# Performance work log

Hardware: AMD Instinct MI355X
Metric: run time of the kernel (lower is better)

The kernel has to match this reference:

```python
import jax, jax.numpy as jnp
import numpy as np

N_NODES = 100000
N_EDGES = 3200000
D_FEAT = 64


def setup_inputs() -> dict:
    key = jax.random.key(0)
    k1, k2, k3 = jax.random.split(key, 3)
    x = jax.random.normal(k1, (N_NODES, D_FEAT), dtype=jnp.float32)
    up_index = jax.random.randint(k2, (2, N_EDGES), 0, N_NODES, dtype=jnp.int64)
    down_index = jax.random.randint(k3, (2, N_EDGES), 0, N_NODES, dtype=jnp.int64)
    return {"x": x, "up_index": up_index, "down_index": down_index}


def _propagate(x, edge_index, num_nodes):
    # flow = 'source_to_target': (i, j) = (1, 0)
    # __lift__: gather x along node_dim=-2 at source indices (row j=0)
    msg = x[edge_index[0]]                      # [E, D]  message_up(x_j) = x_j
    # aggregate 'add': scatter-add messages to target indices (row i=1)
    return jax.ops.segment_sum(msg, edge_index[1], num_segments=num_nodes)  # [N, D]


def reference(x, up_index, down_index):
    up_out = _propagate(x, up_index, x.shape[0])
    down_out = _propagate(x, down_index, x.shape[0])
    # update: combine up and down aggregations (identity update -> sum)
    return up_out + down_out
```

## Files before the change

### kernel.cpp

```cpp
#include <hip/hip_runtime.h>


static constexpr int D = 64;
static constexpr int Q = 16;
static constexpr int NPB = 64;
static constexpr int NPB_SHIFT = 6;
static constexpr int CHUNK = 16384;
static constexpr int CH = 4096;

__global__ void detect_idx_dtype(const int* __restrict__ w, int* __restrict__ flag) {
    int tid = threadIdx.x;
    int v = w[2 * tid + 1];
    unsigned long long m = __ballot(v != 0);
    if (tid == 0) *flag = (m == 0ULL) ? 1 : 0;
}

__device__ __forceinline__ int load_idx(const void* idx, long long i, int is64) {
    return is64 ? (int)((const long long*)idx)[i] : ((const int*)idx)[i];
}

__global__ __launch_bounds__(256) void bucket_hist_kernel(
        const void* __restrict__ up, const void* __restrict__ down,
        int* __restrict__ bcounts, const int* __restrict__ flag, int E, int NB) {
    extern __shared__ int lcnt[];
    const int is64 = *flag;
    for (int i = threadIdx.x; i < NB; i += blockDim.x) lcnt[i] = 0;
    __syncthreads();
    const long long total = 2LL * E;
    const long long stride = (long long)gridDim.x * blockDim.x;
    for (long long e = (long long)blockIdx.x * blockDim.x + threadIdx.x;
         e < total; e += stride) {
        const void* idx = up; long long ee = e;
        if (ee >= E) { idx = down; ee -= E; }
        int dst = load_idx(idx, E + ee, is64);
        atomicAdd(&lcnt[dst >> NPB_SHIFT], 1);
    }
    __syncthreads();
    for (int i = threadIdx.x; i < NB; i += blockDim.x)
        if (lcnt[i]) atomicAdd(&bcounts[i], lcnt[i]);
}

__global__ __launch_bounds__(1024) void scan_kernel(
        const int* __restrict__ counts, int* __restrict__ offsets,
        int* __restrict__ cursors, int NB) {
    __shared__ int sums[1024];
    const int tid = threadIdx.x;
    const int chunk = (NB + 1023) / 1024;
    const int start = tid * chunk;
    const int end = min(start + chunk, NB);
    int s = 0;
    for (int i = start; i < end; i++) s += counts[i];
    sums[tid] = s;
    __syncthreads();
    for (int off = 1; off < 1024; off <<= 1) {
        int t = (tid >= off) ? sums[tid - off] : 0;
        __syncthreads();
        sums[tid] += t;
        __syncthreads();
    }
    int run = (tid == 0) ? 0 : sums[tid - 1];
    for (int i = start; i < end; i++) {
        offsets[i] = run;
        cursors[i] = run;
        run += counts[i];
    }
    if (tid == 1023) offsets[NB] = run;
}

__global__ __launch_bounds__(256) void bucket_scatter_kernel(
        const void* __restrict__ up, const void* __restrict__ down,
        int* __restrict__ gcursor, unsigned* __restrict__ packed,
        const int* __restrict__ flag, int E, int NB) {
    extern __shared__ int lds[];
    int* cnt = lds;
    int* base = lds + NB;
    const int is64 = *flag;
    const long long total = 2LL * E;
    const long long cs = (long long)blockIdx.x * CHUNK;
    if (cs >= total) return;
    const long long ce = min(total, cs + (long long)CHUNK);

    for (int i = threadIdx.x; i < NB; i += blockDim.x) cnt[i] = 0;
    __syncthreads();
    for (long long e = cs + threadIdx.x; e < ce; e += blockDim.x) {
        const void* idx = up; long long ee = e;
        if (ee >= E) { idx = down; ee -= E; }
        int dst = load_idx(idx, E + ee, is64);
        atomicAdd(&cnt[dst >> NPB_SHIFT], 1);
    }
    __syncthreads();
    for (int i = threadIdx.x; i < NB; i += blockDim.x) {
        int c = cnt[i];
        base[i] = c ? atomicAdd(&gcursor[i], c) : 0;
        cnt[i] = 0;
    }
    __syncthreads();
    for (long long e = cs + threadIdx.x; e < ce; e += blockDim.x) {
        const void* idx = up; long long ee = e;
        if (ee >= E) { idx = down; ee -= E; }
        int src = load_idx(idx, ee, is64);
        int dst = load_idx(idx, E + ee, is64);
        int b = dst >> NPB_SHIFT;
        int pos = base[b] + atomicAdd(&cnt[b], 1);
        packed[pos] = ((unsigned)src << NPB_SHIFT) | (unsigned)(dst & (NPB - 1));
    }
}

__global__ __launch_bounds__(256) void bucket_gather_kernel(
        const float* __restrict__ x, const int* __restrict__ offsets,
        const unsigned* __restrict__ packed, float* __restrict__ out, int N) {
    __shared__ unsigned sorted[CH];
    __shared__ int cnt[NPB];
    __shared__ int binoff[NPB + 1];
    __shared__ int cursor[NPB];

    const int b = blockIdx.x;
    const int tid = threadIdx.x;
    const int g = tid >> 4;
    const int q = tid & 15;
    const int beg = offsets[b], end = offsets[b + 1];

    float4 acc[4];
    acc[0] = acc[1] = acc[2] = acc[3] = make_float4(0.f, 0.f, 0.f, 0.f);

    for (int cs = beg; cs < end; cs += CH) {
        const int m = min(CH, end - cs);
        for (int i = tid; i < NPB; i += 256) cnt[i] = 0;
        __syncthreads();
        for (int i = tid; i < m; i += 256)
            atomicAdd(&cnt[packed[cs + i] & (NPB - 1)], 1);
        __syncthreads();
        if (tid < NPB) {
            int v = cnt[tid];
            int inc = v;
            #pragma unroll
            for (int off = 1; off < 64; off <<= 1) {
                int t = __shfl_up(inc, off, 64);
                if (tid >= off) inc += t;
            }
            binoff[tid + 1] = inc;
            cursor[tid] = inc - v;
            if (tid == 0) binoff[0] = 0;
        }
        __syncthreads();
        for (int i = tid; i < m; i += 256) {
            unsigned p = packed[cs + i];
            int pos = atomicAdd(&cursor[p & (NPB - 1)], 1);
            sorted[pos] = p;
        }
        __syncthreads();
        #pragma unroll
        for (int j = 0; j < 4; j++) {
            const int dl = 4 * g + j;
            const int rb = binoff[dl], re = binoff[dl + 1];
            int e = rb;
            for (; e + 3 < re; e += 4) {
                unsigned p0 = sorted[e], p1 = sorted[e + 1];
                unsigned p2 = sorted[e + 2], p3 = sorted[e + 3];
                const float4 v0 = *(const float4*)(x + ((long long)(p0 >> NPB_SHIFT)) * D + q * 4);
                const float4 v1 = *(const float4*)(x + ((long long)(p1 >> NPB_SHIFT)) * D + q * 4);
                const float4 v2 = *(const float4*)(x + ((long long)(p2 >> NPB_SHIFT)) * D + q * 4);
                const float4 v3 = *(const float4*)(x + ((long long)(p3 >> NPB_SHIFT)) * D + q * 4);
                acc[j].x += (v0.x + v1.x) + (v2.x + v3.x);
                acc[j].y += (v0.y + v1.y) + (v2.y + v3.y);
                acc[j].z += (v0.z + v1.z) + (v2.z + v3.z);
                acc[j].w += (v0.w + v1.w) + (v2.w + v3.w);
            }
            for (; e < re; e++) {
                unsigned p = sorted[e];
                const float4 v = *(const float4*)(x + ((long long)(p >> NPB_SHIFT)) * D + q * 4);
                acc[j].x += v.x; acc[j].y += v.y; acc[j].z += v.z; acc[j].w += v.w;
            }
        }
        __syncthreads();
    }

    const int node0 = b * NPB;
    #pragma unroll
    for (int j = 0; j < 4; j++) {
        const int node = node0 + 4 * g + j;
        if (node < N)
            *(float4*)(out + (long long)node * D + q * 4) = acc[j];
    }
}

__global__ __launch_bounds__(256) void scatter_add_kernel(
        const float* __restrict__ x, const void* __restrict__ up_idx,
        const void* __restrict__ down_idx, float* __restrict__ out,
        const int* __restrict__ dtype_flag, int num_edges) {
    const int is64 = *dtype_flag;
    const long long total = 2LL * num_edges * Q;
    const long long stride = (long long)gridDim.x * blockDim.x;
    for (long long t = (long long)blockIdx.x * blockDim.x + threadIdx.x;
         t < total; t += stride) {
        const int quad = (int)(t & (Q - 1));
        long long eg = t >> 4;
        const void* idx = up_idx;
        if (eg >= num_edges) { idx = down_idx; eg -= num_edges; }
        int src = load_idx(idx, eg, is64);
        int dst = load_idx(idx, num_edges + eg, is64);
        const float4 v = *(const float4*)(x + (long long)src * D + quad * 4);
        float* o = out + (long long)dst * D + quad * 4;
        unsafeAtomicAdd(o + 0, v.x);
        unsafeAtomicAdd(o + 1, v.y);
        unsafeAtomicAdd(o + 2, v.z);
        unsafeAtomicAdd(o + 3, v.w);
    }
}

extern "C" void kernel_launch(void* const* d_in, const int* in_sizes, int n_in,
                              void* d_out, int out_size, void* d_ws, size_t ws_size,
                              hipStream_t stream) {
    const float* x = (const float*)d_in[0];
    const void* up_idx = d_in[1];
    const void* down_idx = d_in[2];
    float* out = (float*)d_out;

    const int E = in_sizes[1] / 2;
    const int N = out_size / D;
    const int NB = (N + NPB - 1) / NPB;
    const long long Etot = 2LL * E;

    int* ws_i = (int*)d_ws;
    int* flag = ws_i;
    int* counts = ws_i + 64;
    int* offsets = counts + NB;
    int* cursors = offsets + NB + 15;
    unsigned* packed = (unsigned*)(cursors + NB);
    const size_t ws_need = (size_t)(64 + 3LL * NB + 16 + Etot) * 4 + 64;

    detect_idx_dtype<<<1, 64, 0, stream>>>((const int*)up_idx, flag);

    if (ws_size >= ws_need && N <= (1 << 25) && Etot < (1LL << 31)) {
        hipMemsetAsync(counts, 0, (size_t)NB * sizeof(int), stream);
        bucket_hist_kernel<<<512, 256, NB * sizeof(int), stream>>>(
            up_idx, down_idx, counts, flag, E, NB);
        scan_kernel<<<1, 1024, 0, stream>>>(counts, offsets, cursors, NB);
        const int sblocks = (int)((Etot + CHUNK - 1) / CHUNK);
        bucket_scatter_kernel<<<sblocks, 256, 2 * NB * sizeof(int), stream>>>(
            up_idx, down_idx, cursors, packed, flag, E, NB);
        bucket_gather_kernel<<<NB, 256, 0, stream>>>(x, offsets, packed, out, N);
    } else {
        hipMemsetAsync(d_out, 0, (size_t)out_size * sizeof(float), stream);
        scatter_add_kernel<<<8192, 256, 0, stream>>>(x, up_idx, down_idx, out, flag, E);
    }
}
```

Baseline: 496.5 us.

## Replace bucketed two-level sort with full per-node CSR counting sort

Replaces the 64-node bucket sort and in-block LDS re-sort with a full per-destination counting sort. It histograms with global atomics per node, runs a two-pass multi-block scan, and scatters source indices into CSR order. The gather kernel then reads each node's contiguous source list directly, unrolled by 8, with nontemporal index loads and no shared memory or barriers. This removes the LDS sorting stage and the serial single-block scan, at the cost of heavy contention on global atomics in the hist and scatter passes and a fully random scatter write pattern.

```diff
diff --git a/kernel.cpp b/kernel.cpp
--- a/kernel.cpp
+++ b/kernel.cpp
@@ -3,10 +3,8 @@
 
 static constexpr int D = 64;
 static constexpr int Q = 16;
-static constexpr int NPB = 64;
-static constexpr int NPB_SHIFT = 6;
-static constexpr int CHUNK = 16384;
-static constexpr int CH = 4096;
+static constexpr int NPB = 32;
+static constexpr int SB = 256;
 
 __global__ void detect_idx_dtype(const int* __restrict__ w, int* __restrict__ flag) {
     int tid = threadIdx.x;
@@ -19,13 +17,10 @@
     return is64 ? (int)((const long long*)idx)[i] : ((const int*)idx)[i];
 }
 
-__global__ __launch_bounds__(256) void bucket_hist_kernel(
+__global__ __launch_bounds__(256) void hist_kernel(
         const void* __restrict__ up, const void* __restrict__ down,
-        int* __restrict__ bcounts, const int* __restrict__ flag, int E, int NB) {
-    extern __shared__ int lcnt[];
+        int* __restrict__ counts, const int* __restrict__ flag, int E) {
     const int is64 = *flag;
-    for (int i = threadIdx.x; i < NB; i += blockDim.x) lcnt[i] = 0;
-    __syncthreads();
     const long long total = 2LL * E;
     const long long stride = (long long)gridDim.x * blockDim.x;
     for (long long e = (long long)blockIdx.x * blockDim.x + threadIdx.x;
@@ -33,154 +28,134 @@
         const void* idx = up; long long ee = e;
         if (ee >= E) { idx = down; ee -= E; }
         int dst = load_idx(idx, E + ee, is64);
-        atomicAdd(&lcnt[dst >> NPB_SHIFT], 1);
-    }
-    __syncthreads();
-    for (int i = threadIdx.x; i < NB; i += blockDim.x)
-        if (lcnt[i]) atomicAdd(&bcounts[i], lcnt[i]);
-}
-
-__global__ __launch_bounds__(1024) void scan_kernel(
-        const int* __restrict__ counts, int* __restrict__ offsets,
-        int* __restrict__ cursors, int NB) {
-    __shared__ int sums[1024];
-    const int tid = threadIdx.x;
-    const int chunk = (NB + 1023) / 1024;
-    const int start = tid * chunk;
-    const int end = min(start + chunk, NB);
+        atomicAdd(&counts[dst], 1);
+    }
+}
+
+__global__ __launch_bounds__(256) void scan_partials_kernel(
+        const int* __restrict__ counts, int* __restrict__ partials,
+        int N, int cpt) {
+    __shared__ int red[256];
+    const int blk = blockIdx.x, tid = threadIdx.x;
+    const long long base = (long long)(blk * 256 + tid) * cpt;
     int s = 0;
-    for (int i = start; i < end; i++) s += counts[i];
-    sums[tid] = s;
-    __syncthreads();
-    for (int off = 1; off < 1024; off <<= 1) {
-        int t = (tid >= off) ? sums[tid - off] : 0;
-        __syncthreads();
-        sums[tid] += t;
-        __syncthreads();
-    }
-    int run = (tid == 0) ? 0 : sums[tid - 1];
-    for (int i = start; i < end; i++) {
-        offsets[i] = run;
-        cursors[i] = run;
-        run += counts[i];
-    }
-    if (tid == 1023) offsets[NB] = run;
-}
-
-__global__ __launch_bounds__(256) void bucket_scatter_kernel(
+    for (int k = 0; k < cpt; k++) {
+        long long i = base + k;
+        if (i < N) s += counts[i];
+    }
+    red[tid] = s;
+    __syncthreads();
+    for (int off = 128; off > 0; off >>= 1) {
+        if (tid < off) red[tid] += red[tid + off];
+        __syncthreads();
+    }
+    if (tid == 0) partials[blk] = red[0];
+}
+
+__global__ __launch_bounds__(256) void scan_apply_kernel(
+        const int* __restrict__ counts, const int* __restrict__ partials,
+        int* __restrict__ offsets, int* __restrict__ cursors,
+        int N, int cpt, int total) {
+    __shared__ int sh[256];
+    const int blk = blockIdx.x, tid = threadIdx.x;
+    sh[tid] = (tid < blk) ? partials[tid] : 0;
+    __syncthreads();
+    for (int off = 128; off > 0; off >>= 1) {
+        if (tid < off) sh[tid] += sh[tid + off];
+        __syncthreads();
+    }
+    const int bbase = sh[0];
+    __syncthreads();
+    const long long base = (long long)(blk * 256 + tid) * cpt;
+    int s = 0;
+    for (int k = 0; k < cpt; k++) {
+        long long i = base + k;
+        if (i < N) s += counts[i];
+    }
+    sh[tid] = s;
+    __syncthreads();
+    for (int off = 1; off < 256; off <<= 1) {
+        int t = (tid >= off) ? sh[tid - off] : 0;
+        __syncthreads();
+        sh[tid] += t;
+        __syncthreads();
+    }
+    int run = bbase + ((tid == 0) ? 0 : sh[tid - 1]);
+    for (int k = 0; k < cpt; k++) {
+        long long i = base + k;
+        if (i < N) {
+            int c = counts[i];
+            offsets[i] = run;
+            cursors[i] = run;
+            run += c;
+        }
+    }
+    if (blk == 0 && tid == 0) offsets[N] = total;
+}
+
+__global__ __launch_bounds__(256) void scatter_kernel(
         const void* __restrict__ up, const void* __restrict__ down,
-        int* __restrict__ gcursor, unsigned* __restrict__ packed,
-        const int* __restrict__ flag, int E, int NB) {
-    extern __shared__ int lds[];
-    int* cnt = lds;
-    int* base = lds + NB;
+        int* __restrict__ cursors, int* __restrict__ srcbuf,
+        const int* __restrict__ flag, int E) {
     const int is64 = *flag;
     const long long total = 2LL * E;
-    const long long cs = (long long)blockIdx.x * CHUNK;
-    if (cs >= total) return;
-    const long long ce = min(total, cs + (long long)CHUNK);
-
-    for (int i = threadIdx.x; i < NB; i += blockDim.x) cnt[i] = 0;
-    __syncthreads();
-    for (long long e = cs + threadIdx.x; e < ce; e += blockDim.x) {
-        const void* idx = up; long long ee = e;
-        if (ee >= E) { idx = down; ee -= E; }
-        int dst = load_idx(idx, E + ee, is64);
-        atomicAdd(&cnt[dst >> NPB_SHIFT], 1);
-    }
-    __syncthreads();
-    for (int i = threadIdx.x; i < NB; i += blockDim.x) {
-        int c = cnt[i];
-        base[i] = c ? atomicAdd(&gcursor[i], c) : 0;
-        cnt[i] = 0;
-    }
-    __syncthreads();
-    for (long long e = cs + threadIdx.x; e < ce; e += blockDim.x) {
+    const long long stride = (long long)gridDim.x * blockDim.x;
+    for (long long e = (long long)blockIdx.x * blockDim.x + threadIdx.x;
+         e < total; e += stride) {
         const void* idx = up; long long ee = e;
         if (ee >= E) { idx = down; ee -= E; }
         int src = load_idx(idx, ee, is64);
         int dst = load_idx(idx, E + ee, is64);
-        int b = dst >> NPB_SHIFT;
-        int pos = base[b] + atomicAdd(&cnt[b], 1);
-        packed[pos] = ((unsigned)src << NPB_SHIFT) | (unsigned)(dst & (NPB - 1));
-    }
-}
-
-__global__ __launch_bounds__(256) void bucket_gather_kernel(
+        int pos = atomicAdd(&cursors[dst], 1);
+        __builtin_nontemporal_store(src, &srcbuf[pos]);
+    }
+}
+
+__global__ __launch_bounds__(256, 6) void gather_kernel(
         const float* __restrict__ x, const int* __restrict__ offsets,
-        const unsigned* __restrict__ packed, float* __restrict__ out, int N) {
-    __shared__ unsigned sorted[CH];
-    __shared__ int cnt[NPB];
-    __shared__ int binoff[NPB + 1];
-    __shared__ int cursor[NPB];
-
-    const int b = blockIdx.x;
+        const int* __restrict__ srcs, float* __restrict__ out, int N) {
     const int tid = threadIdx.x;
     const int g = tid >> 4;
     const int q = tid & 15;
-    const int beg = offsets[b], end = offsets[b + 1];
-
-    float4 acc[4];
-    acc[0] = acc[1] = acc[2] = acc[3] = make_float4(0.f, 0.f, 0.f, 0.f);
-
-    for (int cs = beg; cs < end; cs += CH) {
-        const int m = min(CH, end - cs);
-        for (int i = tid; i < NPB; i += 256) cnt[i] = 0;
-        __syncthreads();
-        for (int i = tid; i < m; i += 256)
-            atomicAdd(&cnt[packed[cs + i] & (NPB - 1)], 1);
-        __syncthreads();
-        if (tid < NPB) {
-            int v = cnt[tid];
-            int inc = v;
-            #pragma unroll
-            for (int off = 1; off < 64; off <<= 1) {
-                int t = __shfl_up(inc, off, 64);
-                if (tid >= off) inc += t;
-            }
-            binoff[tid + 1] = inc;
-            cursor[tid] = inc - v;
-            if (tid == 0) binoff[0] = 0;
-        }
-        __syncthreads();
-        for (int i = tid; i < m; i += 256) {
-            unsigned p = packed[cs + i];
-            int pos = atomicAdd(&cursor[p & (NPB - 1)], 1);
-            sorted[pos] = p;
-        }
-        __syncthreads();
-        #pragma unroll
-        for (int j = 0; j < 4; j++) {
-            const int dl = 4 * g + j;
-            const int rb = binoff[dl], re = binoff[dl + 1];
+    const float* xq = x + q * 4;
+
+    #pragma unroll
+    for (int j = 0; j < 2; j++) {
+        const int node = blockIdx.x * NPB + 2 * g + j;
+        if (node < N) {
+            const int rb = offsets[node];
+            const int re = offsets[node + 1];
+            float4 acc = make_float4(0.f, 0.f, 0.f, 0.f);
             int e = rb;
-            for (; e + 3 < re; e += 4) {
-                unsigned p0 = sorted[e], p1 = sorted[e + 1];
-                unsigned p2 = sorted[e + 2], p3 = sorted[e + 3];
-                const float4 v0 = *(const float4*)(x + ((long long)(p0 >> NPB_SHIFT)) * D + q * 4);
-                const float4 v1 = *(const float4*)(x + ((long long)(p1 >> NPB_SHIFT)) * D + q * 4);
-                const float4 v2 = *(const float4*)(x + ((long long)(p2 >> NPB_SHIFT)) * D + q * 4);
-                const float4 v3 = *(const float4*)(x + ((long long)(p3 >> NPB_SHIFT)) * D + q * 4);
-                acc[j].x += (v0.x + v1.x) + (v2.x + v3.x);
-                acc[j].y += (v0.y + v1.y) + (v2.y + v3.y);
-                acc[j].z += (v0.z + v1.z) + (v2.z + v3.z);
-                acc[j].w += (v0.w + v1.w) + (v2.w + v3.w);
+            for (; e + 8 <= re; e += 8) {
+                const int s0 = __builtin_nontemporal_load(srcs + e + 0);
+                const int s1 = __builtin_nontemporal_load(srcs + e + 1);
+                const int s2 = __builtin_nontemporal_load(srcs + e + 2);
+                const int s3 = __builtin_nontemporal_load(srcs + e + 3);
+                const int s4 = __builtin_nontemporal_load(srcs + e + 4);
+                const int s5 = __builtin_nontemporal_load(srcs + e + 5);
+                const int s6 = __builtin_nontemporal_load(srcs + e + 6);
+                const int s7 = __builtin_nontemporal_load(srcs + e + 7);
+                const float4 v0 = *(const float4*)(xq + (long long)s0 * D);
+                const float4 v1 = *(const float4*)(xq + (long long)s1 * D);
+                const float4 v2 = *(const float4*)(xq + (long long)s2 * D);
+                const float4 v3 = *(const float4*)(xq + (long long)s3 * D);
+                const float4 v4 = *(const float4*)(xq + (long long)s4 * D);
+                const float4 v5 = *(const float4*)(xq + (long long)s5 * D);
+                const float4 v6 = *(const float4*)(xq + (long long)s6 * D);
+                const float4 v7 = *(const float4*)(xq + (long long)s7 * D);
+                acc.x += ((v0.x + v1.x) + (v2.x + v3.x)) + ((v4.x + v5.x) + (v6.x + v7.x));
+                acc.y += ((v0.y + v1.y) + (v2.y + v3.y)) + ((v4.y + v5.y) + (v6.y + v7.y));
+                acc.z += ((v0.z + v1.z) + (v2.z + v3.z)) + ((v4.z + v5.z) + (v6.z + v7.z));
+                acc.w += ((v0.w + v1.w) + (v2.w + v3.w)) + ((v4.w + v5.w) + (v6.w + v7.w));
             }
             for (; e < re; e++) {
-                unsigned p = sorted[e];
-                const float4 v = *(const float4*)(x + ((long long)(p >> NPB_SHIFT)) * D + q * 4);
-                acc[j].x += v.x; acc[j].y += v.y; acc[j].z += v.z; acc[j].w += v.w;
+                const int s = __builtin_nontemporal_load(srcs + e);
+                const float4 v = *(const float4*)(xq + (long long)s * D);
+                acc.x += v.x; acc.y += v.y; acc.z += v.z; acc.w += v.w;
             }
+            *(float4*)(out + (long long)node * D + q * 4) = acc;
         }
-        __syncthreads();
-    }
-
-    const int node0 = b * NPB;
-    #pragma unroll
-    for (int j = 0; j < 4; j++) {
-        const int node = node0 + 4 * g + j;
-        if (node < N)
-            *(float4*)(out + (long long)node * D + q * 4) = acc[j];
     }
 }
 
@@ -218,28 +193,29 @@
 
     const int E = in_sizes[1] / 2;
     const int N = out_size / D;
-    const int NB = (N + NPB - 1) / NPB;
     const long long Etot = 2LL * E;
 
     int* ws_i = (int*)d_ws;
     int* flag = ws_i;
     int* counts = ws_i + 64;
-    int* offsets = counts + NB;
-    int* cursors = offsets + NB + 15;
-    unsigned* packed = (unsigned*)(cursors + NB);
-    const size_t ws_need = (size_t)(64 + 3LL * NB + 16 + Etot) * 4 + 64;
+    int* offsets = counts + N;
+    int* cursors = offsets + N + 16;
+    int* partials = cursors + N;
+    int* srcbuf = partials + 320;
+    const size_t ws_need = ((size_t)64 + 3LL * N + 16 + 320 + (size_t)Etot) * 4 + 64;
 
     detect_idx_dtype<<<1, 64, 0, stream>>>((const int*)up_idx, flag);
 
-    if (ws_size >= ws_need && N <= (1 << 25) && Etot < (1LL << 31)) {
-        hipMemsetAsync(counts, 0, (size_t)NB * sizeof(int), stream);
-        bucket_hist_kernel<<<512, 256, NB * sizeof(int), stream>>>(
-            up_idx, down_idx, counts, flag, E, NB);
-        scan_kernel<<<1, 1024, 0, stream>>>(counts, offsets, cursors, NB);
-        const int sblocks = (int)((Etot + CHUNK - 1) / CHUNK);
-        bucket_scatter_kernel<<<sblocks, 256, 2 * NB * sizeof(int), stream>>>(
-            up_idx, down_idx, cursors, packed, flag, E, NB);
-        bucket_gather_kernel<<<NB, 256, 0, stream>>>(x, offsets, packed, out, N);
+    if (ws_size >= ws_need && Etot < (1LL << 31) && N >= 1) {
+        hipMemsetAsync(counts, 0, (size_t)N * sizeof(int), stream);
+        hist_kernel<<<2048, 256, 0, stream>>>(up_idx, down_idx, counts, flag, E);
+        const int cpt = (N + SB * 256 - 1) / (SB * 256);
+        scan_partials_kernel<<<SB, 256, 0, stream>>>(counts, partials, N, cpt);
+        scan_apply_kernel<<<SB, 256, 0, stream>>>(counts, partials, offsets, cursors,
+                                                  N, cpt, (int)Etot);
+        scatter_kernel<<<2048, 256, 0, stream>>>(up_idx, down_idx, cursors, srcbuf,
+                                                 flag, E);
+        gather_kernel<<<(N + NPB - 1) / NPB, 256, 0, stream>>>(x, offsets, srcbuf, out, N);
     } else {
         hipMemsetAsync(d_out, 0, (size_t)out_size * sizeof(float), stream);
         scatter_add_kernel<<<8192, 256, 0, stream>>>(x, up_idx, down_idx, out, flag, E);
```

Measured after the change: 1.154 ms. 132% more time.

## Sub-sort gather edges by source range for locality, use nontemporal index loads

Applied to the files above, without the earlier changes.

The gather kernel now sorts each chunk's edges by (source range tile, destination node) rather than by destination alone, so all blocks read x in source-region order and improve L2 locality. Index and packed loads use nontemporal hints so the streamed data does not pollute cache. The scatter chunk size is halved and the histogram grid doubled to raise parallelism. The costs are extra LDS for NT*64 bins, a more expensive in-block scan, and extra loop overhead per tile.

```diff
diff --git a/kernel.cpp b/kernel.cpp
--- a/kernel.cpp
+++ b/kernel.cpp
@@ -5,8 +5,9 @@
 static constexpr int Q = 16;
 static constexpr int NPB = 64;
 static constexpr int NPB_SHIFT = 6;
-static constexpr int CHUNK = 16384;
+static constexpr int CHUNK = 8192;
 static constexpr int CH = 4096;
+static constexpr int MAXT = 32;
 
 __global__ void detect_idx_dtype(const int* __restrict__ w, int* __restrict__ flag) {
     int tid = threadIdx.x;
@@ -15,8 +16,9 @@
     if (tid == 0) *flag = (m == 0ULL) ? 1 : 0;
 }
 
-__device__ __forceinline__ int load_idx(const void* idx, long long i, int is64) {
-    return is64 ? (int)((const long long*)idx)[i] : ((const int*)idx)[i];
+__device__ __forceinline__ int load_idx_nt(const void* idx, long long i, int is64) {
+    return is64 ? (int)__builtin_nontemporal_load(((const long long*)idx) + i)
+                : __builtin_nontemporal_load(((const int*)idx) + i);
 }
 
 __global__ __launch_bounds__(256) void bucket_hist_kernel(
@@ -32,7 +34,7 @@
          e < total; e += stride) {
         const void* idx = up; long long ee = e;
         if (ee >= E) { idx = down; ee -= E; }
-        int dst = load_idx(idx, E + ee, is64);
+        int dst = load_idx_nt(idx, E + ee, is64);
         atomicAdd(&lcnt[dst >> NPB_SHIFT], 1);
     }
     __syncthreads();
@@ -85,7 +87,7 @@
     for (long long e = cs + threadIdx.x; e < ce; e += blockDim.x) {
         const void* idx = up; long long ee = e;
         if (ee >= E) { idx = down; ee -= E; }
-        int dst = load_idx(idx, E + ee, is64);
+        int dst = load_idx_nt(idx, E + ee, is64);
         atomicAdd(&cnt[dst >> NPB_SHIFT], 1);
     }
     __syncthreads();
@@ -98,8 +100,8 @@
     for (long long e = cs + threadIdx.x; e < ce; e += blockDim.x) {
         const void* idx = up; long long ee = e;
         if (ee >= E) { idx = down; ee -= E; }
-        int src = load_idx(idx, ee, is64);
-        int dst = load_idx(idx, E + ee, is64);
+        int src = load_idx_nt(idx, ee, is64);
+        int dst = load_idx_nt(idx, E + ee, is64);
         int b = dst >> NPB_SHIFT;
         int pos = base[b] + atomicAdd(&cnt[b], 1);
         packed[pos] = ((unsigned)src << NPB_SHIFT) | (unsigned)(dst & (NPB - 1));
@@ -108,68 +110,93 @@
 
 __global__ __launch_bounds__(256) void bucket_gather_kernel(
         const float* __restrict__ x, const int* __restrict__ offsets,
-        const unsigned* __restrict__ packed, float* __restrict__ out, int N) {
-    __shared__ unsigned sorted[CH];
-    __shared__ int cnt[NPB];
-    __shared__ int binoff[NPB + 1];
-    __shared__ int cursor[NPB];
+        const unsigned* __restrict__ packed, float* __restrict__ out,
+        int N, int shift, int NT) {
+    extern __shared__ int lds[];
+    unsigned* sorted = (unsigned*)lds;
+    int* cnt = lds + CH;
+    int* cursor = cnt + NT * NPB;
+    int* binoff = cursor + NT * NPB;
+    const int nbins = NT * NPB;
 
     const int b = blockIdx.x;
     const int tid = threadIdx.x;
     const int g = tid >> 4;
     const int q = tid & 15;
     const int beg = offsets[b], end = offsets[b + 1];
+    const float* xq = x + q * 4;
 
     float4 acc[4];
     acc[0] = acc[1] = acc[2] = acc[3] = make_float4(0.f, 0.f, 0.f, 0.f);
 
     for (int cs = beg; cs < end; cs += CH) {
         const int m = min(CH, end - cs);
-        for (int i = tid; i < NPB; i += 256) cnt[i] = 0;
-        __syncthreads();
-        for (int i = tid; i < m; i += 256)
-            atomicAdd(&cnt[packed[cs + i] & (NPB - 1)], 1);
-        __syncthreads();
-        if (tid < NPB) {
-            int v = cnt[tid];
-            int inc = v;
+        for (int i = tid; i < nbins; i += 256) cnt[i] = 0;
+        __syncthreads();
+        for (int i = tid; i < m; i += 256) {
+            unsigned p = __builtin_nontemporal_load(packed + cs + i);
+            int key = (int)((p >> (NPB_SHIFT + shift)) << NPB_SHIFT) | (int)(p & (NPB - 1));
+            atomicAdd(&cnt[key], 1);
+        }
+        __syncthreads();
+        if (tid < 64) {
+            const int K = (nbins + 63) >> 6;
+            const int base = tid * K;
+            int S = 0;
+            for (int k = 0; k < K; k++) {
+                int i = base + k;
+                if (i < nbins) S += cnt[i];
+            }
+            int inc = S;
             #pragma unroll
             for (int off = 1; off < 64; off <<= 1) {
                 int t = __shfl_up(inc, off, 64);
                 if (tid >= off) inc += t;
             }
-            binoff[tid + 1] = inc;
-            cursor[tid] = inc - v;
+            int run = inc - S;
+            for (int k = 0; k < K; k++) {
+                int i = base + k;
+                if (i < nbins) {
+                    int c = cnt[i];
+                    cursor[i] = run;
+                    binoff[i + 1] = run + c;
+                    run += c;
+                }
+            }
             if (tid == 0) binoff[0] = 0;
         }
         __syncthreads();
         for (int i = tid; i < m; i += 256) {
-            unsigned p = packed[cs + i];
-            int pos = atomicAdd(&cursor[p & (NPB - 1)], 1);
+            unsigned p = __builtin_nontemporal_load(packed + cs + i);
+            int key = (int)((p >> (NPB_SHIFT + shift)) << NPB_SHIFT) | (int)(p & (NPB - 1));
+            int pos = atomicAdd(&cursor[key], 1);
             sorted[pos] = p;
         }
         __syncthreads();
-        #pragma unroll
-        for (int j = 0; j < 4; j++) {
-            const int dl = 4 * g + j;
-            const int rb = binoff[dl], re = binoff[dl + 1];
-            int e = rb;
-            for (; e + 3 < re; e += 4) {
-                unsigned p0 = sorted[e], p1 = sorted[e + 1];
-                unsigned p2 = sorted[e + 2], p3 = sorted[e + 3];
-                const float4 v0 = *(const float4*)(x + ((long long)(p0 >> NPB_SHIFT)) * D + q * 4);
-                const float4 v1 = *(const float4*)(x + ((long long)(p1 >> NPB_SHIFT)) * D + q * 4);
-                const float4 v2 = *(const float4*)(x + ((long long)(p2 >> NPB_SHIFT)) * D + q * 4);
-                const float4 v3 = *(const float4*)(x + ((long long)(p3 >> NPB_SHIFT)) * D + q * 4);
-                acc[j].x += (v0.x + v1.x) + (v2.x + v3.x);
-                acc[j].y += (v0.y + v1.y) + (v2.y + v3.y);
-                acc[j].z += (v0.z + v1.z) + (v2.z + v3.z);
-                acc[j].w += (v0.w + v1.w) + (v2.w + v3.w);
-            }
-            for (; e < re; e++) {
-                unsigned p = sorted[e];
-                const float4 v = *(const float4*)(x + ((long long)(p >> NPB_SHIFT)) * D + q * 4);
-                acc[j].x += v.x; acc[j].y += v.y; acc[j].z += v.z; acc[j].w += v.w;
+        for (int t = 0; t < NT; t++) {
+            #pragma unroll
+            for (int j = 0; j < 4; j++) {
+                const int dl = 4 * g + j;
+                const int key = t * NPB + dl;
+                const int rb = binoff[key], re = binoff[key + 1];
+                int e = rb;
+                for (; e + 3 < re; e += 4) {
+                    unsigned p0 = sorted[e], p1 = sorted[e + 1];
+                    unsigned p2 = sorted[e + 2], p3 = sorted[e + 3];
+                    const float4 v0 = *(const float4*)(xq + ((long long)(p0 >> NPB_SHIFT)) * D);
+                    const float4 v1 = *(const float4*)(xq + ((long long)(p1 >> NPB_SHIFT)) * D);
+                    const float4 v2 = *(const float4*)(xq + ((long long)(p2 >> NPB_SHIFT)) * D);
+                    const float4 v3 = *(const float4*)(xq + ((long long)(p3 >> NPB_SHIFT)) * D);
+                    acc[j].x += (v0.x + v1.x) + (v2.x + v3.x);
+                    acc[j].y += (v0.y + v1.y) + (v2.y + v3.y);
+                    acc[j].z += (v0.z + v1.z) + (v2.z + v3.z);
+                    acc[j].w += (v0.w + v1.w) + (v2.w + v3.w);
+                }
+                for (; e < re; e++) {
+                    unsigned p = sorted[e];
+                    const float4 v = *(const float4*)(xq + ((long long)(p >> NPB_SHIFT)) * D);
+                    acc[j].x += v.x; acc[j].y += v.y; acc[j].z += v.z; acc[j].w += v.w;
+                }
             }
         }
         __syncthreads();
@@ -197,8 +224,8 @@
         long long eg = t >> 4;
         const void* idx = up_idx;
         if (eg >= num_edges) { idx = down_idx; eg -= num_edges; }
-        int src = load_idx(idx, eg, is64);
-        int dst = load_idx(idx, num_edges + eg, is64);
+        int src = load_idx_nt(idx, eg, is64);
+        int dst = load_idx_nt(idx, num_edges + eg, is64);
         const float4 v = *(const float4*)(x + (long long)src * D + quad * 4);
         float* o = out + (long long)dst * D + quad * 4;
         unsafeAtomicAdd(o + 0, v.x);
@@ -221,6 +248,10 @@
     const int NB = (N + NPB - 1) / NPB;
     const long long Etot = 2LL * E;
 
+    int shift = 13;
+    while ((((long long)(N - 1) >> shift) + 1) > MAXT) shift++;
+    const int NT = (int)(((long long)(N - 1) >> shift) + 1);
+
     int* ws_i = (int*)d_ws;
     int* flag = ws_i;
     int* counts = ws_i + 64;
@@ -233,13 +264,16 @@
 
     if (ws_size >= ws_need && N <= (1 << 25) && Etot < (1LL << 31)) {
         hipMemsetAsync(counts, 0, (size_t)NB * sizeof(int), stream);
-        bucket_hist_kernel<<<512, 256, NB * sizeof(int), stream>>>(
+        bucket_hist_kernel<<<1024, 256, NB * sizeof(int), stream>>>(
             up_idx, down_idx, counts, flag, E, NB);
         scan_kernel<<<1, 1024, 0, stream>>>(counts, offsets, cursors, NB);
         const int sblocks = (int)((Etot + CHUNK - 1) / CHUNK);
         bucket_scatter_kernel<<<sblocks, 256, 2 * NB * sizeof(int), stream>>>(
             up_idx, down_idx, cursors, packed, flag, E, NB);
-        bucket_gather_kernel<<<NB, 256, 0, stream>>>(x, offsets, packed, out, N);
+        const int nbins = NT * NPB;
+        const size_t glds = (size_t)CH * 4 + (size_t)(3 * nbins + 1 + 3) * 4;
+        bucket_gather_kernel<<<NB, 256, glds, stream>>>(
+            x, offsets, packed, out, N, shift, NT);
     } else {
         hipMemsetAsync(d_out, 0, (size_t)out_size * sizeof(float), stream);
         scatter_add_kernel<<<8192, 256, 0, stream>>>(x, up_idx, down_idx, out, flag, E);
```

After: 528.4 us. +6.4%, slower.
